# Optimization experiments

Measured on AMD Instinct MI355X. Metric: run time of the kernel, lower is better.

The kernel has to match this reference:

```python
import jax, jax.numpy as jnp
import numpy as np

NUM_BEAMS = 4
EOS = 2
PAD = 0
T = 16  # max_tokens decode steps
NEG = jnp.float32(-1e32)


def setup_inputs() -> dict:
    key = jax.random.key(0)
    ks = jax.random.split(key, 12)
    Vv, E, D, L, bs = 32000, 512, 512, 2, 16
    s = 0.05
    n = lambda k, sh: (jax.random.normal(k, sh, dtype=jnp.float32) * s)
    return {
        'inputs': jax.random.randint(ks[0], (1, bs), 0, Vv),
        'h0': n(ks[1], (L, bs, D)),
        'c0': n(ks[2], (L, bs, D)),
        'emb': n(ks[3], (Vv, E)),
        'Wih0': n(ks[4], (4 * D, E)),
        'Whh0': n(ks[5], (4 * D, D)),
        'b0': n(ks[6], (4 * D,)),
        'Wih1': n(ks[7], (4 * D, D)),
        'Whh1': n(ks[8], (4 * D, D)),
        'b1': n(ks[9], (4 * D,)),
        'Wp': n(ks[10], (D, Vv)),
        'bp': n(ks[11], (Vv,)),
    }


def _lstm(x, h, c, Wih, Whh, b):
    z = x @ Wih.T + h @ Whh.T + b
    i, f, g, o = jnp.split(z, 4, axis=-1)
    c = jax.nn.sigmoid(f) * c + jax.nn.sigmoid(i) * jnp.tanh(g)
    h = jax.nn.sigmoid(o) * jnp.tanh(c)
    return h, c


def reference(inputs, h0, c0, emb, Wih0, Whh0, b0, Wih1, Whh1, b1, Wp, bp):
    bs = inputs.shape[1]
    nb = NUM_BEAMS
    B = bs * nb
    Vv = emb.shape[0]

    def cell(tok, h, c):
        # one decode step of the 2-layer LSTM + projection; tok: (B,)
        x = emb[tok]
        h0n, c0n = _lstm(x, h[0], c[0], Wih0, Whh0, b0)
        h1n, c1n = _lstm(h0n, h[1], c[1], Wih1, Whh1, b1)
        logits = h1n @ Wp + bp  # (B, V)
        return logits, jnp.stack([h0n, h1n]), jnp.stack([c0n, c1n])

    offs = jnp.arange(bs)[:, None] * nb  # batch-major beam layout b*nb+beam

    # ---- iteration 0: all beams identical, keep beam 0 only ----
    tokens = jnp.repeat(inputs[0], nb)           # (B,)
    h = jnp.repeat(h0, nb, axis=1)               # (L, B, D)
    c = jnp.repeat(c0, nb, axis=1)
    logits0, h, c = cell(tokens, h, c)
    lp0 = jax.nn.log_softmax(logits0, axis=-1).reshape(bs, nb, Vv)[:, 0, :]
    logprobs, beams = jax.lax.top_k(lp0, nb)     # (bs, nb)
    pidx = (beams // Vv + offs).reshape(-1)      # parents == 0
    tokens = (beams % Vv).reshape(-1)
    h = h[:, pidx]
    c = c[:, pidx]
    finished = tokens == EOS
    beam_out = jnp.zeros((T + 1, B), dtype=tokens.dtype)
    beam_out = beam_out.at[0].set(jnp.repeat(inputs[0], nb)[pidx]).at[1].set(tokens)

    # ---- iterations 1..T-1 ----
    def step(carry, t):
        tokens, h, c, logprobs, finished, beam_out = carry
        logits, h, c = cell(tokens, h, c)
        new_lp = jax.nn.log_softmax(logits, axis=-1).reshape(bs, nb, Vv) + logprobs[:, :, None]
        # finished beams: forced to emit PAD with unchanged cumulative logprob
        masked = jnp.full((bs, nb, Vv), NEG).at[:, :, PAD].set(logprobs)
        fin = finished.reshape(bs, nb)
        new_lp = jnp.where(fin[:, :, None], masked, new_lp)
        logprobs, beams = jax.lax.top_k(new_lp.reshape(bs, nb * Vv), nb)
        pidx = (beams // Vv + offs).reshape(-1)
        toks = (beams % Vv).reshape(-1)
        h = h[:, pidx]
        c = c[:, pidx]
        finished = finished[pidx] | (toks == EOS)
        beam_out = beam_out[:, pidx].at[t + 1].set(toks)
        return (toks, h, c, logprobs, finished, beam_out), logits

    carry0 = (tokens, h, c, logprobs, finished, beam_out)
    carry_f, logits_seq = jax.lax.scan(step, carry0, jnp.arange(1, T))
    logits_all = jnp.concatenate([logits0[None], logits_seq], axis=0)  # (T, B, V)
    beam_outputs = carry_f[5].reshape(T + 1, bs, nb)
    return logits_all, beam_outputs
```

## Files before the change

### kernel.cpp

```cpp
#include <hip/hip_runtime.h>
#include <math.h>

#define BS     16
#define NB     4
#define BB     64
#define DD     512
#define VV     32000
#define TSTEPS 16
#define EOSTOK 2
#define NEGF   (-1e32f)
#define VT2    32
#define NVT2   (VV / VT2)

__device__ __forceinline__ bool better(float av, int ai, float bv, int bi_) {
    return (av > bv) || (av == bv && ai < bi_);
}

__device__ __forceinline__ void glds4(const float* src, float* dst) {
    __builtin_amdgcn_global_load_lds((const __attribute__((address_space(1))) void*)src,
                                     (__attribute__((address_space(3))) void*)dst, 4, 0, 0);
}
__device__ __forceinline__ void glds16(const float* src, float* dst) {
    __builtin_amdgcn_global_load_lds((const __attribute__((address_space(1))) void*)src,
                                     (__attribute__((address_space(3))) void*)dst, 16, 0, 0);
}

__global__ void init_kernel(const int* __restrict__ inputs,
                            const float* __restrict__ h0, const float* __restrict__ c0,
                            float* __restrict__ h0s, float* __restrict__ c0s,
                            float* __restrict__ h1s, float* __restrict__ c1s,
                            int* __restrict__ tokens, int* __restrict__ pidx,
                            int* __restrict__ fin, float* __restrict__ lp,
                            int* __restrict__ bo)
{
    int tid = blockIdx.x * blockDim.x + threadIdx.x;
    int total = BB * DD;
    for (int i = tid; i < total; i += gridDim.x * blockDim.x) {
        int b = i / DD;
        int d = i % DD;
        int src0 = 0 * BS * DD + (b >> 2) * DD + d;
        int src1 = 1 * BS * DD + (b >> 2) * DD + d;
        h0s[i] = h0[src0];
        c0s[i] = c0[src0];
        h1s[i] = h0[src1];
        c1s[i] = c0[src1];
    }
    if (tid < BB) {
        tokens[tid] = inputs[tid >> 2];
        pidx[tid]   = tid;
        fin[tid]    = 0;
        lp[tid]     = 0.0f;
        bo[0 * BB + tid] = inputs[tid >> 2];
        for (int r = 1; r <= TSTEPS; r++) bo[r * BB + tid] = 0;
    }
}

__global__ __launch_bounds__(128) void lstm_kernel(
    const float* __restrict__ xbase, const int* __restrict__ xrow,
    const float* __restrict__ hsrc,  const float* __restrict__ csrc,
    const int* __restrict__ prow,
    float* __restrict__ hdst, float* __restrict__ cdst,
    const float* __restrict__ Wih, const float* __restrict__ Whh,
    const float* __restrict__ bias)
{
    __shared__ float U[32][129];
    __shared__ float Wl[4][1024];
    __shared__ double Z[4][32];
    __shared__ int rows_s[32], prows_s[32];
    int tid = threadIdx.x;
    int j  = blockIdx.x >> 1;
    int bo_ = (blockIdx.x & 1) * 32;
    int b = tid & 31;
    int g = tid >> 5;
    int lane = tid & 63;
    int w = tid >> 6;

    #pragma unroll
    for (int i = 0; i < 8; i++) {
        int s0 = (i * 2 + w) * 64;
        int gg = s0 >> 8;
        int hh = (s0 >> 7) & 1;
        int c0 = s0 & 127;
        const float* rowbase = (hh ? Whh : Wih) + (size_t)(gg * DD + j) * DD;
        glds16(rowbase + 4 * (c0 + lane), (float*)Wl + 4 * s0);
    }
    if (tid < 32) {
        rows_s[tid]  = xrow ? xrow[bo_ + tid] : (bo_ + tid);
        prows_s[tid] = prow[bo_ + tid];
    }

    double a0 = 0.0, a1 = 0.0, a2 = 0.0, a3 = 0.0;
    for (int ch = 0; ch < 8; ch++) {
        int k0 = ch * 128;
        __syncthreads();
        #pragma unroll
        for (int i = 0; i < 32; i++) {
            int s = i * 2 + w;
            int bb = s >> 1;
            int kk0 = (s & 1) * 64;
            const float* src;
            if (k0 < 512) src = xbase + (size_t)rows_s[bb] * DD + k0 + kk0 + lane;
            else          src = hsrc + (size_t)prows_s[bb] * DD + (k0 - 512) + kk0 + lane;
            glds4(src, &U[bb][kk0]);
        }
        __syncthreads();
        const float* Wrow = &Wl[g][k0];
        #pragma unroll 8
        for (int kk = 0; kk < 128; kk += 4) {
            a0 = fma((double)U[b][kk + 0], (double)Wrow[kk + 0], a0);
            a1 = fma((double)U[b][kk + 1], (double)Wrow[kk + 1], a1);
            a2 = fma((double)U[b][kk + 2], (double)Wrow[kk + 2], a2);
            a3 = fma((double)U[b][kk + 3], (double)Wrow[kk + 3], a3);
        }
    }
    Z[g][b] = ((a0 + a1) + (a2 + a3));
    __syncthreads();

    if (tid < 32) {
        int gb = bo_ + b;
        double zi = Z[0][b] + (double)bias[0 * DD + j];
        double zf = Z[1][b] + (double)bias[1 * DD + j];
        double zg = Z[2][b] + (double)bias[2 * DD + j];
        double zo = Z[3][b] + (double)bias[3 * DD + j];
        double si = 1.0 / (1.0 + exp(-zi));
        double sf = 1.0 / (1.0 + exp(-zf));
        double so = 1.0 / (1.0 + exp(-zo));
        double cold = (double)csrc[(size_t)prows_s[b] * DD + j];
        double cn = sf * cold + si * tanh(zg);
        double hn = so * tanh(cn);
        hdst[gb * DD + j] = (float)hn;
        cdst[gb * DD + j] = (float)cn;
    }
}

__global__ __launch_bounds__(256) void proj_kernel(
    const float* __restrict__ h1, const float* __restrict__ Wp,
    const float* __restrict__ bp, float* __restrict__ outf)
{
    __shared__ float sh[64][68];
    __shared__ float sw[64][32];
    int vbase = blockIdx.x * VT2;
    int tid = threadIdx.x;
    int lane = tid & 63;
    int w = tid >> 6;
    int b0 = (tid >> 4) * 4;
    int v0 = (tid & 15) * 2;

    double acc[4][2];
    #pragma unroll
    for (int i = 0; i < 4; i++) { acc[i][0] = 0.0; acc[i][1] = 0.0; }

    for (int ch = 0; ch < 8; ch++) {
        int k0 = ch * 64;
        __syncthreads();
        #pragma unroll
        for (int i = 0; i < 16; i++) {
            int bb = i * 4 + w;
            glds4(h1 + (size_t)bb * DD + k0 + lane, &sh[bb][0]);
        }
        #pragma unroll
        for (int i = 0; i < 8; i++) {
            int r2 = i * 4 + w;
            const float* src = Wp + (size_t)(k0 + 2 * r2 + (lane >> 5)) * VV
                                  + vbase + (lane & 31);
            glds4(src, &sw[2 * r2][0]);
        }
        __syncthreads();
        #pragma unroll
        for (int k4 = 0; k4 < 16; k4++) {
            int k = k4 * 4;
            float4 h4[4]; float2 w2[4];
            #pragma unroll
            for (int i = 0; i < 4; i++) h4[i] = *(const float4*)&sh[b0 + i][k];
            #pragma unroll
            for (int kk = 0; kk < 4; kk++) w2[kk] = *(const float2*)&sw[k + kk][v0];
            #pragma unroll
            for (int i = 0; i < 4; i++) {
                const float hh[4] = {h4[i].x, h4[i].y, h4[i].z, h4[i].w};
                #pragma unroll
                for (int kk = 0; kk < 4; kk++) {
                    double hd = (double)hh[kk];
                    acc[i][0] = fma(hd, (double)w2[kk].x, acc[i][0]);
                    acc[i][1] = fma(hd, (double)w2[kk].y, acc[i][1]);
                }
            }
        }
    }

    #pragma unroll
    for (int i = 0; i < 4; i++) {
        int brow = b0 + i;
        #pragma unroll
        for (int q = 0; q < 2; q++) {
            int v = vbase + v0 + q;
            outf[(size_t)brow * VV + v] = (float)(acc[i][q] + (double)bp[v]);
        }
    }
}

#define NPT 32
__global__ __launch_bounds__(1024) void row_kernel(
    const float* __restrict__ outf, const float* __restrict__ lp,
    const int* __restrict__ fin,
    float* __restrict__ rcv, int* __restrict__ rci, int step0)
{
    int row = blockIdx.x;
    int j   = row & 3;
    int tid = threadIdx.x;
    int base_idx = j * VV;

    float lp_r = step0 ? 0.0f : lp[row];
    int   f    = step0 ? 0    : fin[row];
    if (step0 && j != 0) {
        if (tid < 4) { rcv[row * 4 + tid] = NEGF; rci[row * 4 + tid] = base_idx + tid; }
        return;
    }
    if (f) {
        if (tid < 4) {
            rcv[row * 4 + tid] = (tid == 0) ? lp_r : NEGF;
            rci[row * 4 + tid] = base_idx + tid;
        }
        return;
    }

    const float* xo = outf + (size_t)row * VV;
    __shared__ double red[1024];

    float zreg[NPT];
    double m = -1e300;
    #pragma unroll
    for (int q = 0; q < NPT; q++) {
        int i = tid + q * 1024;
        float zf = 0.0f;
        if (i < VV) {
            zf = xo[i];
            m = fmax(m, (double)zf);
        }
        zreg[q] = zf;
    }

    red[tid] = m; __syncthreads();
    for (int s = 512; s > 0; s >>= 1) {
        if (tid < s) red[tid] = fmax(red[tid], red[tid + s]);
        __syncthreads();
    }
    m = red[0];
    __syncthreads();

    double sum = 0.0;
    #pragma unroll
    for (int q = 0; q < NPT; q++) {
        int i = tid + q * 1024;
        if (i < VV) sum += exp((double)zreg[q] - m);
    }
    red[tid] = sum; __syncthreads();
    for (int s = 512; s > 0; s >>= 1) {
        if (tid < s) red[tid] += red[tid + s];
        __syncthreads();
    }
    double lse = m + log(red[0]);
    __syncthreads();

    float bv[4]; int bx[4];
    #pragma unroll
    for (int q = 0; q < 4; q++) { bv[q] = -3.4e38f; bx[q] = 0x7fffffff; }
    #pragma unroll
    for (int q = 0; q < NPT; q++) {
        int i = tid + q * 1024;
        if (i < VV) {
            float lgp32 = (float)((double)zreg[q] - lse);
            float val   = (float)((double)lp_r + (double)lgp32);
            int idx = base_idx + i;
            if (better(val, idx, bv[3], bx[3])) {
                bv[3] = val; bx[3] = idx;
                #pragma unroll
                for (int s = 3; s > 0; s--) {
                    if (better(bv[s], bx[s], bv[s - 1], bx[s - 1])) {
                        float tv2 = bv[s]; bv[s] = bv[s - 1]; bv[s - 1] = tv2;
                        int ti2 = bx[s]; bx[s] = bx[s - 1]; bx[s - 1] = ti2;
                    }
                }
            }
        }
    }

    __shared__ float sv[1024][4];
    __shared__ int   si_[1024][4];
    #pragma unroll
    for (int q = 0; q < 4; q++) { sv[tid][q] = bv[q]; si_[tid][q] = bx[q]; }
    __syncthreads();
    for (int s = 512; s > 0; s >>= 1) {
        if (tid < s) {
            float av[4], ov[4], mv[4]; int ai[4], oi[4], mi[4];
            #pragma unroll
            for (int q = 0; q < 4; q++) {
                av[q] = sv[tid][q];     ai[q] = si_[tid][q];
                ov[q] = sv[tid + s][q]; oi[q] = si_[tid + s][q];
            }
            int pa = 0, pb = 0;
            #pragma unroll
            for (int q = 0; q < 4; q++) {
                bool takeA = (pb >= 4) || (pa < 4 && better(av[pa], ai[pa], ov[pb], oi[pb]));
                if (takeA) { mv[q] = av[pa]; mi[q] = ai[pa]; pa++; }
                else       { mv[q] = ov[pb]; mi[q] = oi[pb]; pb++; }
            }
            #pragma unroll
            for (int q = 0; q < 4; q++) { sv[tid][q] = mv[q]; si_[tid][q] = mi[q]; }
        }
        __syncthreads();
    }
    if (tid < 4) {
        rcv[row * 4 + tid] = sv[0][tid];
        rci[row * 4 + tid] = si_[0][tid];
    }
}

__global__ void merge_update_kernel(
    const float* __restrict__ rcv, const int* __restrict__ rci,
    float* __restrict__ lp, int* __restrict__ fin,
    int* __restrict__ tokens, int* __restrict__ pidx,
    int* __restrict__ bo, int t)
{
    int b = threadIdx.x;
    int bi = b >> 2, r = b & 3;

    float cv[16]; int ci[16];
    #pragma unroll
    for (int c = 0; c < 16; c++) { cv[c] = rcv[bi * 16 + c]; ci[c] = rci[bi * 16 + c]; }

    int sel = 0;
    #pragma unroll
    for (int c = 0; c < 16; c++) {
        int rank = 0;
        #pragma unroll
        for (int d = 0; d < 16; d++)
            if (d != c && better(cv[d], ci[d], cv[c], ci[c])) rank++;
        if (rank == r) sel = c;
    }

    float v = cv[sel];
    int flat = ci[sel];
    int q = flat / VV;
    int p = q + bi * 4;
    int tok = flat - q * VV;
    int oldfin = fin[p];
    int col[TSTEPS + 1];
    #pragma unroll
    for (int rr = 0; rr <= TSTEPS; rr++) col[rr] = bo[rr * BB + p];
    __syncthreads();
    #pragma unroll
    for (int rr = 0; rr <= TSTEPS; rr++) bo[rr * BB + b] = col[rr];
    bo[(t + 1) * BB + b] = tok;
    fin[b]    = oldfin | (tok == EOSTOK);
    lp[b]     = v;
    tokens[b] = tok;
    pidx[b]   = p;
}

__global__ void final_kernel(const int* __restrict__ bo, float* __restrict__ out)
{
    int i = blockIdx.x * blockDim.x + threadIdx.x;
    if (i < (TSTEPS + 1) * BB) out[i] = (float)bo[i];
}

extern "C" void kernel_launch(void* const* d_in, const int* in_sizes, int n_in,
                              void* d_out, int out_size, void* d_ws, size_t ws_size,
                              hipStream_t stream)
{
    const int*   inputs = (const int*)d_in[0];
    const float* h0   = (const float*)d_in[1];
    const float* c0   = (const float*)d_in[2];
    const float* emb  = (const float*)d_in[3];
    const float* Wih0 = (const float*)d_in[4];
    const float* Whh0 = (const float*)d_in[5];
    const float* b0   = (const float*)d_in[6];
    const float* Wih1 = (const float*)d_in[7];
    const float* Whh1 = (const float*)d_in[8];
    const float* b1   = (const float*)d_in[9];
    const float* Wp   = (const float*)d_in[10];
    const float* bp   = (const float*)d_in[11];
    float* out = (float*)d_out;

    char* w = (char*)d_ws;
    size_t off = 0;
    auto alloc = [&](size_t bytes) { void* p = w + off; off += (bytes + 255) & ~255ULL; return p; };
    float* h0s[2], *c0s[2], *h1s[2], *c1s[2];
    for (int s = 0; s < 2; s++) {
        h0s[s] = (float*)alloc(BB * DD * 4);
        c0s[s] = (float*)alloc(BB * DD * 4);
        h1s[s] = (float*)alloc(BB * DD * 4);
        c1s[s] = (float*)alloc(BB * DD * 4);
    }
    float* rcv   = (float*)alloc(BB * 4 * 4);
    int*   rci   = (int*)alloc(BB * 4 * 4);
    float* lp    = (float*)alloc(BB * 4);
    int* pidx    = (int*)alloc(BB * 4);
    int* tokens  = (int*)alloc(BB * 4);
    int* fin     = (int*)alloc(BB * 4);
    int* bo      = (int*)alloc((TSTEPS + 1) * BB * 4);

    init_kernel<<<128, 256, 0, stream>>>(inputs, h0, c0,
                                         h0s[0], c0s[0], h1s[0], c1s[0],
                                         tokens, pidx, fin, lp, bo);

    for (int t = 0; t < TSTEPS; t++) {
        int s = t & 1, d2 = s ^ 1;
        lstm_kernel<<<1024, 128, 0, stream>>>(emb, tokens, h0s[s], c0s[s], pidx,
                                              h0s[d2], c0s[d2], Wih0, Whh0, b0);
        lstm_kernel<<<1024, 128, 0, stream>>>(h0s[d2], nullptr, h1s[s], c1s[s], pidx,
                                              h1s[d2], c1s[d2], Wih1, Whh1, b1);

        float* outf = out + (size_t)t * BB * VV;
        proj_kernel<<<NVT2, 256, 0, stream>>>(h1s[d2], Wp, bp, outf);
        row_kernel<<<BB, 1024, 0, stream>>>(outf, lp, fin, rcv, rci, t == 0 ? 1 : 0);
        merge_update_kernel<<<1, 64, 0, stream>>>(rcv, rci, lp, fin, tokens, pidx, bo, t);
    }
    final_kernel<<<5, 256, 0, stream>>>(bo, out + (size_t)TSTEPS * BB * VV);
}
```

Baseline: 2.855 ms.

## Fuse beam merge into row kernel via last-block counter; widen projection tile

Removes the separate single-block merge/update kernel. The last row_kernel block to finish, found with a global atomic counter, now does the 16-candidate ranking and beam state update, which cuts one launch and one dependency per decode step. The projection kernel's vocabulary tile grows from 32 to 64 columns, with 4x4 fp64 accumulators per thread, so each loaded hidden tile is reused across more outputs with half as many blocks. The trade-offs are higher register pressure in the projection kernel and the correctness risk of atomic and threadfence cross-block signalling.

```diff
diff --git a/kernel.cpp b/kernel.cpp
--- a/kernel.cpp
+++ b/kernel.cpp
@@ -9,8 +9,8 @@
 #define TSTEPS 16
 #define EOSTOK 2
 #define NEGF   (-1e32f)
-#define VT2    32
-#define NVT2   (VV / VT2)
+#define VT     64
+#define NVT    (VV / VT)
 
 __device__ __forceinline__ bool better(float av, int ai, float bv, int bi_) {
     return (av > bv) || (av == bv && ai < bi_);
@@ -31,7 +31,7 @@
                             float* __restrict__ h1s, float* __restrict__ c1s,
                             int* __restrict__ tokens, int* __restrict__ pidx,
                             int* __restrict__ fin, float* __restrict__ lp,
-                            int* __restrict__ bo)
+                            int* __restrict__ bo, unsigned int* __restrict__ counter)
 {
     int tid = blockIdx.x * blockDim.x + threadIdx.x;
     int total = BB * DD;
@@ -45,6 +45,7 @@
         h1s[i] = h0[src1];
         c1s[i] = c0[src1];
     }
+    if (tid == 0) *counter = 0u;
     if (tid < BB) {
         tokens[tid] = inputs[tid >> 2];
         pidx[tid]   = tid;
@@ -138,17 +139,19 @@
     const float* __restrict__ bp, float* __restrict__ outf)
 {
     __shared__ float sh[64][68];
-    __shared__ float sw[64][32];
-    int vbase = blockIdx.x * VT2;
+    __shared__ float sw[64][68];
+    int vbase = blockIdx.x * VT;
     int tid = threadIdx.x;
     int lane = tid & 63;
     int w = tid >> 6;
     int b0 = (tid >> 4) * 4;
-    int v0 = (tid & 15) * 2;
-
-    double acc[4][2];
+    int v0 = (tid & 15) * 4;
+
+    double acc[4][4];
     #pragma unroll
-    for (int i = 0; i < 4; i++) { acc[i][0] = 0.0; acc[i][1] = 0.0; }
+    for (int i = 0; i < 4; i++)
+        #pragma unroll
+        for (int q = 0; q < 4; q++) acc[i][q] = 0.0;
 
     for (int ch = 0; ch < 8; ch++) {
         int k0 = ch * 64;
@@ -159,29 +162,29 @@
             glds4(h1 + (size_t)bb * DD + k0 + lane, &sh[bb][0]);
         }
         #pragma unroll
-        for (int i = 0; i < 8; i++) {
-            int r2 = i * 4 + w;
-            const float* src = Wp + (size_t)(k0 + 2 * r2 + (lane >> 5)) * VV
-                                  + vbase + (lane & 31);
-            glds4(src, &sw[2 * r2][0]);
+        for (int i = 0; i < 16; i++) {
+            int kk = i * 4 + w;
+            glds4(Wp + (size_t)(k0 + kk) * VV + vbase + lane, &sw[kk][0]);
         }
         __syncthreads();
         #pragma unroll
         for (int k4 = 0; k4 < 16; k4++) {
             int k = k4 * 4;
-            float4 h4[4]; float2 w2[4];
+            float4 h4[4], w4[4];
             #pragma unroll
             for (int i = 0; i < 4; i++) h4[i] = *(const float4*)&sh[b0 + i][k];
             #pragma unroll
-            for (int kk = 0; kk < 4; kk++) w2[kk] = *(const float2*)&sw[k + kk][v0];
+            for (int kk = 0; kk < 4; kk++) w4[kk] = *(const float4*)&sw[k + kk][v0];
             #pragma unroll
             for (int i = 0; i < 4; i++) {
                 const float hh[4] = {h4[i].x, h4[i].y, h4[i].z, h4[i].w};
                 #pragma unroll
                 for (int kk = 0; kk < 4; kk++) {
                     double hd = (double)hh[kk];
-                    acc[i][0] = fma(hd, (double)w2[kk].x, acc[i][0]);
-                    acc[i][1] = fma(hd, (double)w2[kk].y, acc[i][1]);
+                    const float ww[4] = {w4[kk].x, w4[kk].y, w4[kk].z, w4[kk].w};
+                    #pragma unroll
+                    for (int q = 0; q < 4; q++)
+                        acc[i][q] = fma(hd, (double)ww[q], acc[i][q]);
                 }
             }
         }
@@ -191,7 +194,7 @@
     for (int i = 0; i < 4; i++) {
         int brow = b0 + i;
         #pragma unroll
-        for (int q = 0; q < 2; q++) {
+        for (int q = 0; q < 4; q++) {
             int v = vbase + v0 + q;
             outf[(size_t)brow * VV + v] = (float)(acc[i][q] + (double)bp[v]);
         }
@@ -202,159 +205,178 @@
 __global__ __launch_bounds__(1024) void row_kernel(
     const float* __restrict__ outf, const float* __restrict__ lp,
     const int* __restrict__ fin,
-    float* __restrict__ rcv, int* __restrict__ rci, int step0)
-{
+    float* __restrict__ rcv, int* __restrict__ rci,
+    int* __restrict__ tokens, int* __restrict__ pidx, int* __restrict__ bo,
+    unsigned int* __restrict__ counter, int t)
+{
+    int step0 = (t == 0) ? 1 : 0;
     int row = blockIdx.x;
     int j   = row & 3;
     int tid = threadIdx.x;
     int base_idx = j * VV;
 
+    __shared__ float winv[4];
+    __shared__ int   win[4];
+    __shared__ double red[1024];
+
     float lp_r = step0 ? 0.0f : lp[row];
     int   f    = step0 ? 0    : fin[row];
-    if (step0 && j != 0) {
-        if (tid < 4) { rcv[row * 4 + tid] = NEGF; rci[row * 4 + tid] = base_idx + tid; }
-        return;
-    }
-    if (f) {
+
+    bool trivial = (step0 && j != 0) || (!step0 && f);
+    if (trivial) {
         if (tid < 4) {
-            rcv[row * 4 + tid] = (tid == 0) ? lp_r : NEGF;
-            rci[row * 4 + tid] = base_idx + tid;
-        }
-        return;
-    }
-
-    const float* xo = outf + (size_t)row * VV;
-    __shared__ double red[1024];
-
-    float zreg[NPT];
-    double m = -1e300;
-    #pragma unroll
-    for (int q = 0; q < NPT; q++) {
-        int i = tid + q * 1024;
-        float zf = 0.0f;
-        if (i < VV) {
-            zf = xo[i];
-            m = fmax(m, (double)zf);
-        }
-        zreg[q] = zf;
-    }
-
-    red[tid] = m; __syncthreads();
-    for (int s = 512; s > 0; s >>= 1) {
-        if (tid < s) red[tid] = fmax(red[tid], red[tid + s]);
-        __syncthreads();
-    }
-    m = red[0];
-    __syncthreads();
-
-    double sum = 0.0;
-    #pragma unroll
-    for (int q = 0; q < NPT; q++) {
-        int i = tid + q * 1024;
-        if (i < VV) sum += exp((double)zreg[q] - m);
-    }
-    red[tid] = sum; __syncthreads();
-    for (int s = 512; s > 0; s >>= 1) {
-        if (tid < s) red[tid] += red[tid + s];
-        __syncthreads();
-    }
-    double lse = m + log(red[0]);
-    __syncthreads();
-
-    float bv[4]; int bx[4];
-    #pragma unroll
-    for (int q = 0; q < 4; q++) { bv[q] = -3.4e38f; bx[q] = 0x7fffffff; }
-    #pragma unroll
-    for (int q = 0; q < NPT; q++) {
-        int i = tid + q * 1024;
-        if (i < VV) {
-            float lgp32 = (float)((double)zreg[q] - lse);
-            float val   = (float)((double)lp_r + (double)lgp32);
-            int idx = base_idx + i;
-            if (better(val, idx, bv[3], bx[3])) {
-                bv[3] = val; bx[3] = idx;
-                #pragma unroll
-                for (int s = 3; s > 0; s--) {
-                    if (better(bv[s], bx[s], bv[s - 1], bx[s - 1])) {
-                        float tv2 = bv[s]; bv[s] = bv[s - 1]; bv[s - 1] = tv2;
-                        int ti2 = bx[s]; bx[s] = bx[s - 1]; bx[s - 1] = ti2;
+            winv[tid] = ((!step0 && f) && tid == 0) ? lp_r : NEGF;
+            win[tid]  = base_idx + tid;
+        }
+    } else {
+        const float* xo = outf + (size_t)row * VV;
+
+        float zreg[NPT];
+        double m = -1e300;
+        #pragma unroll
+        for (int q = 0; q < NPT; q++) {
+            int i = tid + q * 1024;
+            float zf = 0.0f;
+            if (i < VV) {
+                zf = xo[i];
+                m = fmax(m, (double)zf);
+            }
+            zreg[q] = zf;
+        }
+
+        red[tid] = m; __syncthreads();
+        for (int s = 512; s > 0; s >>= 1) {
+            if (tid < s) red[tid] = fmax(red[tid], red[tid + s]);
+            __syncthreads();
+        }
+        m = red[0];
+        __syncthreads();
+
+        double sum = 0.0;
+        #pragma unroll
+        for (int q = 0; q < NPT; q++) {
+            int i = tid + q * 1024;
+            if (i < VV) sum += exp((double)zreg[q] - m);
+        }
+        red[tid] = sum; __syncthreads();
+        for (int s = 512; s > 0; s >>= 1) {
+            if (tid < s) red[tid] += red[tid + s];
+            __syncthreads();
+        }
+        double lse = m + log(red[0]);
+        __syncthreads();
+
+        float bv[4]; int bx[4];
+        #pragma unroll
+        for (int q = 0; q < 4; q++) { bv[q] = -3.4e38f; bx[q] = 0x7fffffff; }
+        #pragma unroll
+        for (int q = 0; q < NPT; q++) {
+            int i = tid + q * 1024;
+            if (i < VV) {
+                float lgp32 = (float)((double)zreg[q] - lse);
+                float val   = (float)((double)lp_r + (double)lgp32);
+                int idx = base_idx + i;
+                if (better(val, idx, bv[3], bx[3])) {
+                    bv[3] = val; bx[3] = idx;
+                    #pragma unroll
+                    for (int s = 3; s > 0; s--) {
+                        if (better(bv[s], bx[s], bv[s - 1], bx[s - 1])) {
+                            float tv2 = bv[s]; bv[s] = bv[s - 1]; bv[s - 1] = tv2;
+                            int ti2 = bx[s]; bx[s] = bx[s - 1]; bx[s - 1] = ti2;
+                        }
                     }
                 }
             }
         }
-    }
-
-    __shared__ float sv[1024][4];
-    __shared__ int   si_[1024][4];
-    #pragma unroll
-    for (int q = 0; q < 4; q++) { sv[tid][q] = bv[q]; si_[tid][q] = bx[q]; }
+
+        __shared__ float sv[1024][4];
+        __shared__ int   si_[1024][4];
+        #pragma unroll
+        for (int q = 0; q < 4; q++) { sv[tid][q] = bv[q]; si_[tid][q] = bx[q]; }
+        __syncthreads();
+        for (int s = 512; s > 0; s >>= 1) {
+            if (tid < s) {
+                float av[4], ov[4], mv[4]; int ai[4], oi[4], mi[4];
+                #pragma unroll
+                for (int q = 0; q < 4; q++) {
+                    av[q] = sv[tid][q];     ai[q] = si_[tid][q];
+                    ov[q] = sv[tid + s][q]; oi[q] = si_[tid + s][q];
+                }
+                int pa = 0, pb = 0;
+                #pragma unroll
+                for (int q = 0; q < 4; q++) {
+                    bool takeA = (pb >= 4) || (pa < 4 && better(av[pa], ai[pa], ov[pb], oi[pb]));
+                    if (takeA) { mv[q] = av[pa]; mi[q] = ai[pa]; pa++; }
+                    else       { mv[q] = ov[pb]; mi[q] = oi[pb]; pb++; }
+                }
+                #pragma unroll
+                for (int q = 0; q < 4; q++) { sv[tid][q] = mv[q]; si_[tid][q] = mi[q]; }
+            }
+            __syncthreads();
+        }
+        if (tid < 4) { winv[tid] = sv[0][tid]; win[tid] = si_[0][tid]; }
+    }
     __syncthreads();
-    for (int s = 512; s > 0; s >>= 1) {
-        if (tid < s) {
-            float av[4], ov[4], mv[4]; int ai[4], oi[4], mi[4];
-            #pragma unroll
-            for (int q = 0; q < 4; q++) {
-                av[q] = sv[tid][q];     ai[q] = si_[tid][q];
-                ov[q] = sv[tid + s][q]; oi[q] = si_[tid + s][q];
-            }
-            int pa = 0, pb = 0;
-            #pragma unroll
-            for (int q = 0; q < 4; q++) {
-                bool takeA = (pb >= 4) || (pa < 4 && better(av[pa], ai[pa], ov[pb], oi[pb]));
-                if (takeA) { mv[q] = av[pa]; mi[q] = ai[pa]; pa++; }
-                else       { mv[q] = ov[pb]; mi[q] = oi[pb]; pb++; }
-            }
-            #pragma unroll
-            for (int q = 0; q < 4; q++) { sv[tid][q] = mv[q]; si_[tid][q] = mi[q]; }
-        }
-        __syncthreads();
-    }
+
     if (tid < 4) {
-        rcv[row * 4 + tid] = sv[0][tid];
-        rci[row * 4 + tid] = si_[0][tid];
-    }
-}
-
-__global__ void merge_update_kernel(
-    const float* __restrict__ rcv, const int* __restrict__ rci,
-    float* __restrict__ lp, int* __restrict__ fin,
-    int* __restrict__ tokens, int* __restrict__ pidx,
-    int* __restrict__ bo, int t)
-{
-    int b = threadIdx.x;
-    int bi = b >> 2, r = b & 3;
-
-    float cv[16]; int ci[16];
-    #pragma unroll
-    for (int c = 0; c < 16; c++) { cv[c] = rcv[bi * 16 + c]; ci[c] = rci[bi * 16 + c]; }
-
-    int sel = 0;
-    #pragma unroll
-    for (int c = 0; c < 16; c++) {
-        int rank = 0;
-        #pragma unroll
-        for (int d = 0; d < 16; d++)
-            if (d != c && better(cv[d], ci[d], cv[c], ci[c])) rank++;
-        if (rank == r) sel = c;
-    }
-
-    float v = cv[sel];
-    int flat = ci[sel];
-    int q = flat / VV;
-    int p = q + bi * 4;
-    int tok = flat - q * VV;
-    int oldfin = fin[p];
-    int col[TSTEPS + 1];
-    #pragma unroll
-    for (int rr = 0; rr <= TSTEPS; rr++) col[rr] = bo[rr * BB + p];
+        atomicExch((unsigned int*)&rcv[row * 4 + tid], __float_as_uint(winv[tid]));
+        atomicExch((unsigned int*)&rci[row * 4 + tid], (unsigned int)win[tid]);
+        __threadfence();
+    }
     __syncthreads();
-    #pragma unroll
-    for (int rr = 0; rr <= TSTEPS; rr++) bo[rr * BB + b] = col[rr];
-    bo[(t + 1) * BB + b] = tok;
-    fin[b]    = oldfin | (tok == EOSTOK);
-    lp[b]     = v;
-    tokens[b] = tok;
-    pidx[b]   = p;
+
+    __shared__ int lastFlag;
+    if (tid == 0) {
+        unsigned int prev = atomicAdd(counter, 1u);
+        lastFlag = (prev == (unsigned int)(BB - 1)) ? 1 : 0;
+    }
+    __syncthreads();
+    if (!lastFlag) return;
+
+    {
+        int b = tid;
+        int bi = b >> 2, r = b & 3;
+        float vv = 0.0f; int flat = 0, p = 0, tok = 0, oldfin = 0;
+        int col[TSTEPS + 1];
+        bool act = (tid < 64);
+        if (act) {
+            float cv[16]; int ci[16];
+            #pragma unroll
+            for (int c = 0; c < 16; c++) {
+                cv[c] = __uint_as_float(atomicAdd((unsigned int*)&rcv[bi * 16 + c], 0u));
+                ci[c] = (int)atomicAdd((unsigned int*)&rci[bi * 16 + c], 0u);
+            }
+            int sel = 0;
+            #pragma unroll
+            for (int c = 0; c < 16; c++) {
+                int rank = 0;
+                #pragma unroll
+                for (int d = 0; d < 16; d++)
+                    if (d != c && better(cv[d], ci[d], cv[c], ci[c])) rank++;
+                if (rank == r) sel = c;
+            }
+            vv = cv[sel];
+            flat = ci[sel];
+            int q = flat / VV;
+            p = q + bi * 4;
+            tok = flat - q * VV;
+            oldfin = fin[p];
+            #pragma unroll
+            for (int rr = 0; rr <= TSTEPS; rr++) col[rr] = bo[rr * BB + p];
+        }
+        __syncthreads();
+        if (act) {
+            #pragma unroll
+            for (int rr = 0; rr <= TSTEPS; rr++) bo[rr * BB + b] = col[rr];
+            bo[(t + 1) * BB + b] = tok;
+            ((int*)fin)[b] = oldfin | (tok == EOSTOK);
+            ((float*)lp)[b] = vv;
+            tokens[b] = tok;
+            pidx[b]   = p;
+        }
+        __syncthreads();
+        if (tid == 0) atomicExch(counter, 0u);
+    }
 }
 
 __global__ void final_kernel(const int* __restrict__ bo, float* __restrict__ out)
@@ -398,10 +420,11 @@
     int* tokens  = (int*)alloc(BB * 4);
     int* fin     = (int*)alloc(BB * 4);
     int* bo      = (int*)alloc((TSTEPS + 1) * BB * 4);
+    unsigned int* counter = (unsigned int*)alloc(256);
 
     init_kernel<<<128, 256, 0, stream>>>(inputs, h0, c0,
                                          h0s[0], c0s[0], h1s[0], c1s[0],
-                                         tokens, pidx, fin, lp, bo);
+                                         tokens, pidx, fin, lp, bo, counter);
 
     for (int t = 0; t < TSTEPS; t++) {
         int s = t & 1, d2 = s ^ 1;
@@ -411,9 +434,9 @@
                                               h1s[d2], c1s[d2], Wih1, Whh1, b1);
 
         float* outf = out + (size_t)t * BB * VV;
-        proj_kernel<<<NVT2, 256, 0, stream>>>(h1s[d2], Wp, bp, outf);
-        row_kernel<<<BB, 1024, 0, stream>>>(outf, lp, fin, rcv, rci, t == 0 ? 1 : 0);
-        merge_update_kernel<<<1, 64, 0, stream>>>(rcv, rci, lp, fin, tokens, pidx, bo, t);
+        proj_kernel<<<NVT, 256, 0, stream>>>(h1s[d2], Wp, bp, outf);
+        row_kernel<<<BB, 1024, 0, stream>>>(outf, lp, fin, rcv, rci,
+                                            tokens, pidx, bo, counter, t);
     }
     final_kernel<<<5, 256, 0, stream>>>(bo, out + (size_t)TSTEPS * BB * VV);
 }
```

Measured after the change: 2.708 ms. 5.1% less time.
